# Performance work log

Hardware: AMD Instinct MI355X
Metric: run time of the kernel (lower is better)

## Reference

```python
import jax, jax.numpy as jnp
import numpy as np

N_HEADS = 16
D_HEAD = 64
N_ROTATE = 32
ROPE_BASE = 10000.0
MAX_LEN = 2048  # round_up_to_multiple_of_256(keep count); static for jit
BATCH, SEQ = 2, 4096


def setup_inputs() -> dict:
    key = jax.random.key(0)
    kq, kk, kv = jax.random.split(key, 3)
    q = jax.random.normal(kq, (BATCH, N_HEADS, MAX_LEN, D_HEAD), jnp.float32)
    k = jax.random.normal(kk, (BATCH, N_HEADS, SEQ, D_HEAD), jnp.float32)
    v = jax.random.normal(kv, (BATCH, N_HEADS, SEQ, D_HEAD), jnp.float32)
    # causal full mask [batch, seq, seq] and full position ids [batch, seq]
    mask_full = jnp.broadcast_to(jnp.tril(jnp.ones((SEQ, SEQ), bool)), (BATCH, SEQ, SEQ))
    pos_full = jnp.broadcast_to(jnp.arange(SEQ, dtype=jnp.int32), (BATCH, SEQ))
    # skip_mask: exactly MAX_LEN kept tokens per row (random positions)
    rng = np.random.default_rng(0)
    sm = np.zeros((BATCH, SEQ), dtype=bool)
    for i in range(BATCH):
        sm[i, rng.permutation(SEQ)[:MAX_LEN]] = True
    return {"q": q, "k": k, "v": v, "mask_full": mask_full,
            "pos_full": pos_full, "skip_mask": jnp.asarray(sm)}


def _rope_rotate(x, pos):
    # x: [b, h, L, n_rotate], pos: [b, L]
    half = N_ROTATE // 2
    inv_freq = 1.0 / (ROPE_BASE ** (jnp.arange(0, N_ROTATE, 2, dtype=jnp.float32) / N_ROTATE))
    freqs = pos.astype(jnp.float32)[..., None] * inv_freq          # [b, L, half]
    emb = jnp.concatenate([freqs, freqs], axis=-1)[:, None]        # [b, 1, L, n_rotate]
    cos, sin = jnp.cos(emb), jnp.sin(emb)
    x1, x2 = x[..., :half], x[..., half:]
    rot = jnp.concatenate([-x2, x1], axis=-1)                      # rotate_half
    return x * cos + rot * sin


def reference(q, k, v, mask_full, pos_full, skip_mask):
    b, S = skip_mask.shape
    lengths = skip_mask.sum(axis=1)
    # vectorized _trim_attention_mask: stable argsort compacts kept indices to the front
    order = jnp.argsort(jnp.where(skip_mask, 0, 1), axis=1, stable=True)
    idx = order[:, :MAX_LEN]                                       # [b, max_len]
    brow = jnp.arange(b)[:, None]
    mask_trim = mask_full[brow, idx]                               # [b, max_len, S]
    pos_trim = pos_full[brow, idx]                                 # [b, max_len]
    valid = jnp.arange(MAX_LEN)[None, :] < lengths[:, None]
    mask_trim = mask_trim & valid[..., None]
    pos_trim = jnp.where(valid, pos_trim, 0)

    # partial RoPE on first n_rotate channels
    rq = _rope_rotate(q[..., :N_ROTATE], pos_trim)
    rk = _rope_rotate(k[..., :N_ROTATE], pos_full)
    q = jnp.concatenate([rq, q[..., N_ROTATE:]], axis=-1)
    k = jnp.concatenate([rk, k[..., N_ROTATE:]], axis=-1)

    # masked SDPA (bool mask broadcast over heads)
    scale = 1.0 / jnp.sqrt(jnp.float32(D_HEAD))
    scores = jnp.einsum('bhqd,bhkd->bhqk', q, k) * scale
    scores = jnp.where(mask_trim[:, None], scores, jnp.finfo(scores.dtype).min)
    attn = jax.nn.softmax(scores, axis=-1)
    return jnp.einsum('bhqk,bhkd->bhqd', attn, v)
```

## Files before the change

### kernel.cpp

```cpp
#include <hip/hip_runtime.h>
#include <math.h>

#define BB 2
#define HH 16
#define QQ 2048
#define SS 4096
#define DD 64
#define NRH 16
#define NQT128 16

typedef unsigned short u16;
typedef unsigned int   u32;
typedef short bhalf8 __attribute__((ext_vector_type(8)));
typedef float f32x4  __attribute__((ext_vector_type(4)));

typedef __attribute__((address_space(1))) const u32 gu32;
typedef __attribute__((address_space(3))) u32 lu32;

#if __has_builtin(__builtin_amdgcn_exp2f)
#define EXP2(x) __builtin_amdgcn_exp2f(x)
#else
#define EXP2(x) exp2f(x)
#endif

union Frag16 { uint4 u; bhalf8 v; u16 s[8]; uint2 d[2]; };

__device__ __forceinline__ u16 f2bf(float f) {
  union { float f; u32 u; } c; c.f = f;
  return (u16)((c.u + 0x7FFFu + ((c.u >> 16) & 1u)) >> 16);
}

__device__ __forceinline__ u32 cvt_pk_bf16(float lo, float hi) {
  u32 r;
  asm("v_cvt_pk_bf16_f32 %0, %1, %2" : "=v"(r) : "v"(lo), "v"(hi));
  return r;
}

__device__ __forceinline__ bhalf8 ldfrag(const u16* p) {
  Frag16 f; f.u = *reinterpret_cast<const uint4*>(p); return f.v;
}

__device__ __forceinline__ void rope32(float* x, int pos) {
  const float step = 0.8304820237218405f;
  const float fp = (float)pos;
#pragma unroll
  for (int i = 0; i < NRH; ++i) {
    float ang = fp * exp2f(-step * (float)i);
    float sv, cv;
    __sincosf(ang, &sv, &cv);
    float a = x[i], b = x[i + NRH];
    x[i]       = a * cv - b * sv;
    x[i + NRH] = b * cv + a * sv;
  }
}

__global__ void prep_idx_kernel(const unsigned char* __restrict__ sm,
                                int* __restrict__ idx) {
  __shared__ int wsum[4];
  __shared__ int modes;
  const int tid = threadIdx.x;
  const int b = (int)blockIdx.x;

  int c = 0;
  for (int i = 0; i < 32; ++i) c += (sm[tid * 32 + i] != 0) ? 1 : 0;
#pragma unroll
  for (int off = 32; off; off >>= 1) c += __shfl_down(c, off);
  if ((tid & 63) == 0) wsum[tid >> 6] = c;
  __syncthreads();
  if (tid == 0) modes = (wsum[0] + wsum[1] + wsum[2] + wsum[3] > 3000) ? 1 : 0;
  __syncthreads();
  const bool byteMode = (modes != 0);
  const u32* sm32 = (const u32*)sm;

  const int base = b * SS + tid * 16;
  u32 flags = 0;
  for (int i = 0; i < 16; ++i) {
    bool f = byteMode ? (sm[base + i] != 0) : (sm32[base + i] != 0);
    flags |= ((u32)(f ? 1 : 0)) << i;
  }
  int cnt = __popc(flags);
  int vv = cnt;
#pragma unroll
  for (int off = 1; off < 64; off <<= 1) {
    int t = __shfl_up(vv, off);
    if ((tid & 63) >= off) vv += t;
  }
  __syncthreads();
  if ((tid & 63) == 63) wsum[tid >> 6] = vv;
  __syncthreads();
  int add = 0;
  for (int w2 = 0; w2 < (tid >> 6); ++w2) add += wsum[w2];
  int p = vv - cnt + add;
  for (int i = 0; i < 16; ++i) {
    if (flags & (1u << i)) {
      if (p < QQ) idx[b * QQ + p] = tid * 16 + i;
      ++p;
    }
  }
}

__global__ __launch_bounds__(256) void prep_kv_kernel(const float* __restrict__ k,
                                                      const float* __restrict__ v,
                                                      u16* __restrict__ kbf,
                                                      u16* __restrict__ vt) {
  __shared__ u16 tile[64][72];
  if (blockIdx.x < 512) {
    int r = blockIdx.x * 256 + threadIdx.x;
    int pos = r & (SS - 1);
    float x[64];
    const float4* src = (const float4*)(k + (size_t)r * DD);
#pragma unroll
    for (int i = 0; i < 16; ++i) {
      float4 t = src[i];
      x[4 * i] = t.x; x[4 * i + 1] = t.y; x[4 * i + 2] = t.z; x[4 * i + 3] = t.w;
    }
    rope32(x, pos);
    u16 tmp[64];
#pragma unroll
    for (int i = 0; i < 64; ++i) tmp[i] = f2bf(x[i]);
    uint4* dst = (uint4*)(kbf + (size_t)r * DD);
#pragma unroll
    for (int i = 0; i < 8; ++i) dst[i] = ((uint4*)tmp)[i];
  } else {
    int blk = (int)blockIdx.x - 512;
    int bh = blk >> 6;
    int jt = blk & 63;
    int t = threadIdx.x;
    int jl = t >> 2;
    int dc = (t & 3) * 16;
    const float4* src = (const float4*)(v + ((size_t)(bh * SS + jt * 64 + jl)) * DD + dc);
#pragma unroll
    for (int i = 0; i < 4; ++i) {
      float4 f = src[i];
      tile[jl][dc + 4 * i]     = f2bf(f.x);
      tile[jl][dc + 4 * i + 1] = f2bf(f.y);
      tile[jl][dc + 4 * i + 2] = f2bf(f.z);
      tile[jl][dc + 4 * i + 3] = f2bf(f.w);
    }
    __syncthreads();
    int d = t >> 2;
    int c = t & 3;
    u16 o[16];
#pragma unroll
    for (int m = 0; m < 16; ++m)
      o[m] = tile[4 * c + (m >> 2) + ((m & 3) << 4)][d];
    uint4* dst = (uint4*)(vt + ((size_t)(bh * DD + d)) * SS + jt * 64 + c * 16);
    dst[0] = ((uint4*)o)[0];
    dst[1] = ((uint4*)o)[1];
  }
}

__device__ __forceinline__ void stage_tiles(const char* kb_bh, const char* vt_bh,
                                            u16* Kb, u16* Vb, int t0,
                                            int w, int srow, int schk) {
#pragma unroll
  for (int p2 = 0; p2 < 2; ++p2) {
    const int rr = w * 16 + p2 * 8 + srow;
    {
      const char* g = kb_bh + (size_t)(t0 + rr) * 128 + ((schk ^ (rr & 7)) * 16);
      lu32* l = (lu32*)((char*)Kb + (w * 16 + p2 * 8) * 128);
      __builtin_amdgcn_global_load_lds((gu32*)g, l, 16, 0, 0);
    }
    {
      const char* g = vt_bh + (size_t)rr * (SS * 2) + t0 * 2 + ((schk ^ (rr & 7)) * 16);
      lu32* l = (lu32*)((char*)Vb + (w * 16 + p2 * 8) * 128);
      __builtin_amdgcn_global_load_lds((gu32*)g, l, 16, 0, 0);
    }
  }
}

template <bool MASKED>
__device__ __forceinline__ void attn_tile(
    const u16* __restrict__ Kb, const u16* __restrict__ Vb, u16* __restrict__ pb,
    int t0, int grp, int col,
    int bndA0, int bndA1, int bndA2, int bndA3,
    int bndB0, int bndB1, int bndB2, int bndB3,
    int paA0, int paA1, int paB0, int paB1,
    int pwA0, int pwA1, int pwA2, int pwA3,
    int pwB0, int pwB1, int pwB2, int pwB3,
    bhalf8 qaA0, bhalf8 qaA1, bhalf8 qaB0, bhalf8 qaB1,
    f32x4& accA0, f32x4& accA1, f32x4& accA2, f32x4& accA3,
    f32x4& accB0, f32x4& accB1, f32x4& accB2, f32x4& accB3,
    float& lA0, float& lA1, float& lA2, float& lA3,
    float& lB0, float& lB1, float& lB2, float& lB3) {
  const int swz = col & 7;
  f32x4 z = {0.f, 0.f, 0.f, 0.f};
  f32x4 sA0 = z, sA1 = z, sA2 = z, sA3 = z;
  f32x4 sB0 = z, sB1 = z, sB2 = z, sB3 = z;
  {
    const u16* kr0 = Kb + (0 * 16 + col) * 64;
    const u16* kr1 = Kb + (1 * 16 + col) * 64;
    const u16* kr2 = Kb + (2 * 16 + col) * 64;
    const u16* kr3 = Kb + (3 * 16 + col) * 64;
    __builtin_amdgcn_s_setprio(1);
    bhalf8 b0 = ldfrag(kr0 + ((grp ^ swz) * 8));
    sA0 = __builtin_amdgcn_mfma_f32_16x16x32_bf16(qaA0, b0, sA0, 0, 0, 0);
    sB0 = __builtin_amdgcn_mfma_f32_16x16x32_bf16(qaB0, b0, sB0, 0, 0, 0);
    bhalf8 b1 = ldfrag(kr1 + ((grp ^ swz) * 8));
    sA1 = __builtin_amdgcn_mfma_f32_16x16x32_bf16(qaA0, b1, sA1, 0, 0, 0);
    sB1 = __builtin_amdgcn_mfma_f32_16x16x32_bf16(qaB0, b1, sB1, 0, 0, 0);
    bhalf8 b2 = ldfrag(kr2 + ((grp ^ swz) * 8));
    sA2 = __builtin_amdgcn_mfma_f32_16x16x32_bf16(qaA0, b2, sA2, 0, 0, 0);
    sB2 = __builtin_amdgcn_mfma_f32_16x16x32_bf16(qaB0, b2, sB2, 0, 0, 0);
    bhalf8 b3 = ldfrag(kr3 + ((grp ^ swz) * 8));
    sA3 = __builtin_amdgcn_mfma_f32_16x16x32_bf16(qaA0, b3, sA3, 0, 0, 0);
    sB3 = __builtin_amdgcn_mfma_f32_16x16x32_bf16(qaB0, b3, sB3, 0, 0, 0);
    bhalf8 c0 = ldfrag(kr0 + (((4 + grp) ^ swz) * 8));
    sA0 = __builtin_amdgcn_mfma_f32_16x16x32_bf16(qaA1, c0, sA0, 0, 0, 0);
    sB0 = __builtin_amdgcn_mfma_f32_16x16x32_bf16(qaB1, c0, sB0, 0, 0, 0);
    bhalf8 c1 = ldfrag(kr1 + (((4 + grp) ^ swz) * 8));
    sA1 = __builtin_amdgcn_mfma_f32_16x16x32_bf16(qaA1, c1, sA1, 0, 0, 0);
    sB1 = __builtin_amdgcn_mfma_f32_16x16x32_bf16(qaB1, c1, sB1, 0, 0, 0);
    bhalf8 c2 = ldfrag(kr2 + (((4 + grp) ^ swz) * 8));
    sA2 = __builtin_amdgcn_mfma_f32_16x16x32_bf16(qaA1, c2, sA2, 0, 0, 0);
    sB2 = __builtin_amdgcn_mfma_f32_16x16x32_bf16(qaB1, c2, sB2, 0, 0, 0);
    bhalf8 c3 = ldfrag(kr3 + (((4 + grp) ^ swz) * 8));
    sA3 = __builtin_amdgcn_mfma_f32_16x16x32_bf16(qaA1, c3, sA3, 0, 0, 0);
    sB3 = __builtin_amdgcn_mfma_f32_16x16x32_bf16(qaB1, c3, sB3, 0, 0, 0);
    __builtin_amdgcn_s_setprio(0);
  }

  const int key0 = t0 + col;
#define SM_ROW(S0, S1, S2, S3, R, BND, LACC, PWI)                              \
  {                                                                            \
    float p0, p1, p2v, p3;                                                     \
    if (MASKED) {                                                              \
      p0  = (key0      <= (BND)) ? EXP2(S0[R] - 16.f) : 0.f;                   \
      p1  = (key0 + 16 <= (BND)) ? EXP2(S1[R] - 16.f) : 0.f;                   \
      p2v = (key0 + 32 <= (BND)) ? EXP2(S2[R] - 16.f) : 0.f;                   \
      p3  = (key0 + 48 <= (BND)) ? EXP2(S3[R] - 16.f) : 0.f;                   \
    } else {                                                                   \
      p0  = EXP2(S0[R] - 16.f);                                                \
      p1  = EXP2(S1[R] - 16.f);                                                \
      p2v = EXP2(S2[R] - 16.f);                                                \
      p3  = EXP2(S3[R] - 16.f);                                                \
    }                                                                          \
    (LACC) += (p0 + p1) + (p2v + p3);                                          \
    uint2 pw;                                                                  \
    pw.x = cvt_pk_bf16(p0, p1);                                                \
    pw.y = cvt_pk_bf16(p2v, p3);                                               \
    *(uint2*)(pb + (PWI)) = pw;                                                \
  }
  SM_ROW(sA0, sA1, sA2, sA3, 0, bndA0, lA0, pwA0)
  SM_ROW(sA0, sA1, sA2, sA3, 1, bndA1, lA1, pwA1)
  SM_ROW(sA0, sA1, sA2, sA3, 2, bndA2, lA2, pwA2)
  SM_ROW(sA0, sA1, sA2, sA3, 3, bndA3, lA3, pwA3)
  SM_ROW(sB0, sB1, sB2, sB3, 0, bndB0, lB0, pwB0)
  SM_ROW(sB0, sB1, sB2, sB3, 1, bndB1, lB1, pwB1)
  SM_ROW(sB0, sB1, sB2, sB3, 2, bndB2, lB2, pwB2)
  SM_ROW(sB0, sB1, sB2, sB3, 3, bndB3, lB3, pwB3)
#undef SM_ROW

  asm volatile("s_waitcnt lgkmcnt(0)" ::: "memory");
  __builtin_amdgcn_sched_barrier(0);

  bhalf8 paA_0, paA_1, paB_0, paB_1;
  {
    Frag16 f0, f1, g0, g1;
    f0.u = *(const uint4*)(pb + paA0);
    f1.u = *(const uint4*)(pb + paA1);
    g0.u = *(const uint4*)(pb + paB0);
    g1.u = *(const uint4*)(pb + paB1);
    paA_0 = f0.v; paA_1 = f1.v; paB_0 = g0.v; paB_1 = g1.v;
  }

  {
    const u16* vr0 = Vb + (0 * 16 + col) * 64;
    const u16* vr1 = Vb + (1 * 16 + col) * 64;
    const u16* vr2 = Vb + (2 * 16 + col) * 64;
    const u16* vr3 = Vb + (3 * 16 + col) * 64;
    __builtin_amdgcn_s_setprio(1);
    bhalf8 v0 = ldfrag(vr0 + ((grp ^ swz) * 8));
    accA0 = __builtin_amdgcn_mfma_f32_16x16x32_bf16(paA_0, v0, accA0, 0, 0, 0);
    accB0 = __builtin_amdgcn_mfma_f32_16x16x32_bf16(paB_0, v0, accB0, 0, 0, 0);
    bhalf8 v1 = ldfrag(vr1 + ((grp ^ swz) * 8));
    accA1 = __builtin_amdgcn_mfma_f32_16x16x32_bf16(paA_0, v1, accA1, 0, 0, 0);
    accB1 = __builtin_amdgcn_mfma_f32_16x16x32_bf16(paB_0, v1, accB1, 0, 0, 0);
    bhalf8 v2 = ldfrag(vr2 + ((grp ^ swz) * 8));
    accA2 = __builtin_amdgcn_mfma_f32_16x16x32_bf16(paA_0, v2, accA2, 0, 0, 0);
    accB2 = __builtin_amdgcn_mfma_f32_16x16x32_bf16(paB_0, v2, accB2, 0, 0, 0);
    bhalf8 v3 = ldfrag(vr3 + ((grp ^ swz) * 8));
    accA3 = __builtin_amdgcn_mfma_f32_16x16x32_bf16(paA_0, v3, accA3, 0, 0, 0);
    accB3 = __builtin_amdgcn_mfma_f32_16x16x32_bf16(paB_0, v3, accB3, 0, 0, 0);
    bhalf8 u0 = ldfrag(vr0 + (((4 + grp) ^ swz) * 8));
    accA0 = __builtin_amdgcn_mfma_f32_16x16x32_bf16(paA_1, u0, accA0, 0, 0, 0);
    accB0 = __builtin_amdgcn_mfma_f32_16x16x32_bf16(paB_1, u0, accB0, 0, 0, 0);
    bhalf8 u1 = ldfrag(vr1 + (((4 + grp) ^ swz) * 8));
    accA1 = __builtin_amdgcn_mfma_f32_16x16x32_bf16(paA_1, u1, accA1, 0, 0, 0);
    accB1 = __builtin_amdgcn_mfma_f32_16x16x32_bf16(paB_1, u1, accB1, 0, 0, 0);
    bhalf8 u2 = ldfrag(vr2 + (((4 + grp) ^ swz) * 8));
    accA2 = __builtin_amdgcn_mfma_f32_16x16x32_bf16(paA_1, u2, accA2, 0, 0, 0);
    accB2 = __builtin_amdgcn_mfma_f32_16x16x32_bf16(paB_1, u2, accB2, 0, 0, 0);
    bhalf8 u3 = ldfrag(vr3 + (((4 + grp) ^ swz) * 8));
    accA3 = __builtin_amdgcn_mfma_f32_16x16x32_bf16(paA_1, u3, accA3, 0, 0, 0);
    accB3 = __builtin_amdgcn_mfma_f32_16x16x32_bf16(paB_1, u3, accB3, 0, 0, 0);
    __builtin_amdgcn_s_setprio(0);
  }
}

__global__ __launch_bounds__(256) void attn_mfma_kernel(
    const float* __restrict__ qsrc, const u16* __restrict__ kbf,
    const u16* __restrict__ vt, const int* __restrict__ idx,
    float* __restrict__ out) {
  __shared__ u16 KbufA[64 * 64];
  __shared__ u16 VbufA[64 * 64];
  __shared__ u16 KbufB[64 * 64];
  __shared__ u16 VbufB[64 * 64];
  __shared__ __align__(16) u16 Pbuf[4][32 * 64];

  const int blk = (int)blockIdx.x;
  const int bh  = blk & 31;
  const int rank = blk >> 5;
  const int qt  = (rank < 8) ? (15 - 2 * rank) : (2 * (rank - 8));
  const int q0  = qt * 128;
  const int b   = bh >> 4;
  const int tid  = threadIdx.x;
  const int w    = tid >> 6;
  const int lane = tid & 63;
  const int grp  = lane >> 4;
  const int col  = lane & 15;

  const char* kb_bh = (const char*)(kbf + (size_t)bh * SS * DD);
  const char* vt_bh = (const char*)(vt + (size_t)bh * DD * SS);

  const int srow = lane >> 3;
  const int schk = lane & 7;

  u16* pb = Pbuf[w];

  const int* idxb = idx + b * QQ + q0;
  const int bndA0 = idxb[w * 32 + grp * 4 + 0];
  const int bndA1 = idxb[w * 32 + grp * 4 + 1];
  const int bndA2 = idxb[w * 32 + grp * 4 + 2];
  const int bndA3 = idxb[w * 32 + grp * 4 + 3];
  const int bndB0 = idxb[w * 32 + 16 + grp * 4 + 0];
  const int bndB1 = idxb[w * 32 + 16 + grp * 4 + 1];
  const int bndB2 = idxb[w * 32 + 16 + grp * 4 + 2];
  const int bndB3 = idxb[w * 32 + 16 + grp * 4 + 3];
  const int wave_minb = idxb[w * 32];
  const int wave_maxb = idxb[w * 32 + 31];
  const int maxbound  = idxb[127];
  const int ntiles = (maxbound >> 6) + 1;

  const int paA0 = col * 64 + ((grp ^ (col & 7)) << 3);
  const int paA1 = col * 64 + (((grp + 4) ^ (col & 7)) << 3);
  const int paB0 = (16 + col) * 64 + ((grp ^ (col & 7)) << 3);
  const int paB1 = (16 + col) * 64 + (((grp + 4) ^ (col & 7)) << 3);
  const int qg = grp * 4;
  const int pwA0 = (qg + 0) * 64 + ((((col >> 1) ^ ((qg + 0) & 7))) << 3) + ((col & 1) << 2);
  const int pwA1 = (qg + 1) * 64 + ((((col >> 1) ^ ((qg + 1) & 7))) << 3) + ((col & 1) << 2);
  const int pwA2 = (qg + 2) * 64 + ((((col >> 1) ^ ((qg + 2) & 7))) << 3) + ((col & 1) << 2);
  const int pwA3 = (qg + 3) * 64 + ((((col >> 1) ^ ((qg + 3) & 7))) << 3) + ((col & 1) << 2);
  const int pwB0 = (16 + qg + 0) * 64 + ((((col >> 1) ^ ((qg + 0) & 7))) << 3) + ((col & 1) << 2);
  const int pwB1 = (16 + qg + 1) * 64 + ((((col >> 1) ^ ((qg + 1) & 7))) << 3) + ((col & 1) << 2);
  const int pwB2 = (16 + qg + 2) * 64 + ((((col >> 1) ^ ((qg + 2) & 7))) << 3) + ((col & 1) << 2);
  const int pwB3 = (16 + qg + 3) * 64 + ((((col >> 1) ^ ((qg + 3) & 7))) << 3) + ((col & 1) << 2);

  bhalf8 qaA0, qaA1, qaB0, qaB1;
  {
    const int qrow = q0 + w * 32 + col;
    const int mypos = idx[b * QQ + qrow];
    const float* qr = qsrc + (size_t)(bh * QQ + qrow) * DD;
    const int lof = (grp & 1) * 8;
    float4 A0 = *(const float4*)(qr + lof);
    float4 A1 = *(const float4*)(qr + lof + 4);
    float4 B0 = *(const float4*)(qr + 16 + lof);
    float4 B1 = *(const float4*)(qr + 16 + lof + 4);
    float4 C0 = *(const float4*)(qr + 32 + grp * 8);
    float4 C1 = *(const float4*)(qr + 32 + grp * 8 + 4);
    float xlo[8] = {A0.x, A0.y, A0.z, A0.w, A1.x, A1.y, A1.z, A1.w};
    float xhi[8] = {B0.x, B0.y, B0.z, B0.w, B1.x, B1.y, B1.z, B1.w};
    float xq1[8] = {C0.x, C0.y, C0.z, C0.w, C1.x, C1.y, C1.z, C1.w};
    const float scq = 0.125f * 1.44269504088896f;
    const float fp = (float)mypos;
    Frag16 f0, f1;
#pragma unroll
    for (int j = 0; j < 8; ++j) {
      float ang = fp * exp2f(-0.8304820237218405f * (float)(lof + j));
      float sv, cv;
      __sincosf(ang, &sv, &cv);
      float val = (grp >= 2) ? (xhi[j] * cv + xlo[j] * sv)
                             : (xlo[j] * cv - xhi[j] * sv);
      f0.s[j] = f2bf(val * scq);
      f1.s[j] = f2bf(xq1[j] * scq);
    }
    qaA0 = f0.v; qaA1 = f1.v;
  }
  {
    const int qrow = q0 + w * 32 + 16 + col;
    const int mypos = idx[b * QQ + qrow];
    const float* qr = qsrc + (size_t)(bh * QQ + qrow) * DD;
    const int lof = (grp & 1) * 8;
    float4 A0 = *(const float4*)(qr + lof);
    float4 A1 = *(const float4*)(qr + lof + 4);
    float4 B0 = *(const float4*)(qr + 16 + lof);
    float4 B1 = *(const float4*)(qr + 16 + lof + 4);
    float4 C0 = *(const float4*)(qr + 32 + grp * 8);
    float4 C1 = *(const float4*)(qr + 32 + grp * 8 + 4);
    float xlo[8] = {A0.x, A0.y, A0.z, A0.w, A1.x, A1.y, A1.z, A1.w};
    float xhi[8] = {B0.x, B0.y, B0.z, B0.w, B1.x, B1.y, B1.z, B1.w};
    float xq1[8] = {C0.x, C0.y, C0.z, C0.w, C1.x, C1.y, C1.z, C1.w};
    const float scq = 0.125f * 1.44269504088896f;
    const float fp = (float)mypos;
    Frag16 f0, f1;
#pragma unroll
    for (int j = 0; j < 8; ++j) {
      float ang = fp * exp2f(-0.8304820237218405f * (float)(lof + j));
      float sv, cv;
      __sincosf(ang, &sv, &cv);
      float val = (grp >= 2) ? (xhi[j] * cv + xlo[j] * sv)
                             : (xlo[j] * cv - xhi[j] * sv);
      f0.s[j] = f2bf(val * scq);
      f1.s[j] = f2bf(xq1[j] * scq);
    }
    qaB0 = f0.v; qaB1 = f1.v;
  }

  f32x4 z = {0.f, 0.f, 0.f, 0.f};
  f32x4 accA0 = z, accA1 = z, accA2 = z, accA3 = z;
  f32x4 accB0 = z, accB1 = z, accB2 = z, accB3 = z;
  float lA0 = 0.f, lA1 = 0.f, lA2 = 0.f, lA3 = 0.f;
  float lB0 = 0.f, lB1 = 0.f, lB2 = 0.f, lB3 = 0.f;

#define ATTN_CALL(M, KB, VB, T0)                                               \
  attn_tile<M>(KB, VB, pb, T0, grp, col,                                       \
               bndA0, bndA1, bndA2, bndA3, bndB0, bndB1, bndB2, bndB3,         \
               paA0, paA1, paB0, paB1,                                         \
               pwA0, pwA1, pwA2, pwA3, pwB0, pwB1, pwB2, pwB3,                 \
               qaA0, qaA1, qaB0, qaB1,                                         \
               accA0, accA1, accA2, accA3, accB0, accB1, accB2, accB3,         \
               lA0, lA1, lA2, lA3, lB0, lB1, lB2, lB3)

  stage_tiles(kb_bh, vt_bh, KbufA, VbufA, 0, w, srow, schk);
  __syncthreads();

  for (int ti = 0; ti < ntiles; ti += 2) {
    const bool has1 = (ti + 1) < ntiles;
    if (has1) stage_tiles(kb_bh, vt_bh, KbufB, VbufB, (ti + 1) << 6, w, srow, schk);
    {
      const int t0 = ti << 6;
      if (t0 <= wave_maxb) {
        if (t0 + 63 <= wave_minb) ATTN_CALL(false, KbufA, VbufA, t0);
        else                      ATTN_CALL(true,  KbufA, VbufA, t0);
      }
    }
    __syncthreads();
    if (has1) {
      if (ti + 2 < ntiles)
        stage_tiles(kb_bh, vt_bh, KbufA, VbufA, (ti + 2) << 6, w, srow, schk);
      {
        const int t0 = (ti + 1) << 6;
        if (t0 <= wave_maxb) {
          if (t0 + 63 <= wave_minb) ATTN_CALL(false, KbufB, VbufB, t0);
          else                      ATTN_CALL(true,  KbufB, VbufB, t0);
        }
      }
      __syncthreads();
    }
  }
#undef ATTN_CALL

#pragma unroll
  for (int mdel = 1; mdel < 16; mdel <<= 1) {
    lA0 += __shfl_xor(lA0, mdel);
    lA1 += __shfl_xor(lA1, mdel);
    lA2 += __shfl_xor(lA2, mdel);
    lA3 += __shfl_xor(lA3, mdel);
    lB0 += __shfl_xor(lB0, mdel);
    lB1 += __shfl_xor(lB1, mdel);
    lB2 += __shfl_xor(lB2, mdel);
    lB3 += __shfl_xor(lB3, mdel);
  }
  {
    float i0 = 1.f / lA0, i1 = 1.f / lA1, i2 = 1.f / lA2, i3 = 1.f / lA3;
    float* ob = out + (size_t)(bh * QQ + q0 + w * 32 + grp * 4) * DD + col;
#pragma unroll
    for (int r = 0; r < 4; ++r) {
      float iv = (r == 0) ? i0 : (r == 1) ? i1 : (r == 2) ? i2 : i3;
      ob[(size_t)r * DD + 0]  = accA0[r] * iv;
      ob[(size_t)r * DD + 16] = accA1[r] * iv;
      ob[(size_t)r * DD + 32] = accA2[r] * iv;
      ob[(size_t)r * DD + 48] = accA3[r] * iv;
    }
  }
  {
    float i0 = 1.f / lB0, i1 = 1.f / lB1, i2 = 1.f / lB2, i3 = 1.f / lB3;
    float* ob = out + (size_t)(bh * QQ + q0 + w * 32 + 16 + grp * 4) * DD + col;
#pragma unroll
    for (int r = 0; r < 4; ++r) {
      float iv = (r == 0) ? i0 : (r == 1) ? i1 : (r == 2) ? i2 : i3;
      ob[(size_t)r * DD + 0]  = accB0[r] * iv;
      ob[(size_t)r * DD + 16] = accB1[r] * iv;
      ob[(size_t)r * DD + 32] = accB2[r] * iv;
      ob[(size_t)r * DD + 48] = accB3[r] * iv;
    }
  }
}

__global__ __launch_bounds__(64) void attn_fb_kernel(const float* __restrict__ q,
                                                     const float* __restrict__ ksrc,
                                                     const float* __restrict__ v,
                                                     const int* __restrict__ idx,
                                                     float* __restrict__ out) {
  int t = (int)(gridDim.x - 1u - blockIdx.x);
  int sub = t >> 5;
  int bh = t & 31;
  int b = bh >> 4;
  int lane = threadIdx.x;
  int qi = sub * 64 + lane;
  const int bound = idx[b * QQ + qi];

  float qreg[64];
  {
    const float4* qp = (const float4*)(q + ((size_t)bh * QQ + qi) * DD);
#pragma unroll
    for (int i = 0; i < 16; ++i) {
      float4 t4 = qp[i];
      qreg[4 * i] = t4.x; qreg[4 * i + 1] = t4.y;
      qreg[4 * i + 2] = t4.z; qreg[4 * i + 3] = t4.w;
    }
  }
  rope32(qreg, bound);
#pragma unroll
  for (int i = 0; i < 64; ++i) qreg[i] *= 0.125f;

  const float* kbase = ksrc + (size_t)bh * SS * DD;
  const float* vbase = v + (size_t)bh * SS * DD;
  float acc[64];
#pragma unroll
  for (int i = 0; i < 64; ++i) acc[i] = 0.f;
  float mrun = -INFINITY, lrun = 0.f;

  for (int j = 0; j <= bound; ++j) {
    float ka[64];
    const float4* kp = (const float4*)(kbase + (size_t)j * DD);
#pragma unroll
    for (int i = 0; i < 16; ++i) {
      float4 t4 = kp[i];
      ka[4 * i] = t4.x; ka[4 * i + 1] = t4.y;
      ka[4 * i + 2] = t4.z; ka[4 * i + 3] = t4.w;
    }
    rope32(ka, j);
    float s0 = 0.f, s1 = 0.f, s2 = 0.f, s3 = 0.f;
#pragma unroll
    for (int i = 0; i < 16; ++i) {
      s0 = fmaf(qreg[4 * i], ka[4 * i], s0);
      s1 = fmaf(qreg[4 * i + 1], ka[4 * i + 1], s1);
      s2 = fmaf(qreg[4 * i + 2], ka[4 * i + 2], s2);
      s3 = fmaf(qreg[4 * i + 3], ka[4 * i + 3], s3);
    }
    float sc = (s0 + s1) + (s2 + s3);
    if (sc > mrun) {
      float alpha = __expf(mrun - sc);
      lrun *= alpha;
#pragma unroll
      for (int i = 0; i < 64; ++i) acc[i] *= alpha;
      mrun = sc;
    }
    float pw = __expf(sc - mrun);
    lrun += pw;
    const float4* vp = (const float4*)(vbase + (size_t)j * DD);
#pragma unroll
    for (int i = 0; i < 16; ++i) {
      float4 t4 = vp[i];
      acc[4 * i] = fmaf(pw, t4.x, acc[4 * i]);
      acc[4 * i + 1] = fmaf(pw, t4.y, acc[4 * i + 1]);
      acc[4 * i + 2] = fmaf(pw, t4.z, acc[4 * i + 2]);
      acc[4 * i + 3] = fmaf(pw, t4.w, acc[4 * i + 3]);
    }
  }
  float inv = 1.0f / lrun;
  float4* op = (float4*)(out + ((size_t)bh * QQ + qi) * DD);
#pragma unroll
  for (int i = 0; i < 16; ++i) {
    float4 t4;
    t4.x = acc[4 * i] * inv; t4.y = acc[4 * i + 1] * inv;
    t4.z = acc[4 * i + 2] * inv; t4.w = acc[4 * i + 3] * inv;
    op[i] = t4;
  }
}

extern "C" void kernel_launch(void* const* d_in, const int* in_sizes, int n_in,
                              void* d_out, int out_size, void* d_ws, size_t ws_size,
                              hipStream_t stream) {
  (void)in_sizes; (void)n_in; (void)out_size;
  const float* q = (const float*)d_in[0];
  const float* k = (const float*)d_in[1];
  const float* v = (const float*)d_in[2];
  const unsigned char* skip = (const unsigned char*)d_in[5];
  float* out = (float*)d_out;

  char* base = (char*)d_ws;
  int* idx = (int*)base;
  const size_t kbytes = (size_t)BB * HH * SS * DD * 2;
  u16* kbf = (u16*)(base + 16384);
  u16* vtb = (u16*)(base + 16384 + kbytes);
  const size_t need = 16384 + 2 * kbytes;

  prep_idx_kernel<<<2, 256, 0, stream>>>(skip, idx);
  if (ws_size >= need) {
    prep_kv_kernel<<<512 + BB * HH * 64, 256, 0, stream>>>(k, v, kbf, vtb);
    attn_mfma_kernel<<<NQT128 * 32, 256, 0, stream>>>(q, kbf, vtb, idx, out);
  } else {
    attn_fb_kernel<<<1024, 64, 0, stream>>>(q, k, v, idx, out);
  }
}
```

Before: 305.0 us.

## Triple-buffer K/V tiles with explicit vmcnt waits and raw barriers

Adds a third LDS buffer pair for K/V and restructures the main loop into a rotating three-stage pipeline that prefetches two tiles ahead. Full __syncthreads is replaced by partial s_waitcnt vmcnt counts plus s_barrier, so loads for later tiles stay in flight while the current tile is computed. This relies on stage_tiles issuing direct global-to-LDS loads with a fixed count per stage, and it uses more LDS per block, which may reduce occupancy.

```diff
diff --git a/kernel.cpp b/kernel.cpp
--- a/kernel.cpp
+++ b/kernel.cpp
@@ -306,6 +306,8 @@
   __shared__ u16 VbufA[64 * 64];
   __shared__ u16 KbufB[64 * 64];
   __shared__ u16 VbufB[64 * 64];
+  __shared__ u16 KbufC[64 * 64];
+  __shared__ u16 VbufC[64 * 64];
   __shared__ __align__(16) u16 Pbuf[4][32 * 64];
 
   const int blk = (int)blockIdx.x;
@@ -431,32 +433,39 @@
                accA0, accA1, accA2, accA3, accB0, accB1, accB2, accB3,         \
                lA0, lA1, lA2, lA3, lB0, lB1, lB2, lB3)
 
-  stage_tiles(kb_bh, vt_bh, KbufA, VbufA, 0, w, srow, schk);
-  __syncthreads();
-
-  for (int ti = 0; ti < ntiles; ti += 2) {
-    const bool has1 = (ti + 1) < ntiles;
-    if (has1) stage_tiles(kb_bh, vt_bh, KbufB, VbufB, (ti + 1) << 6, w, srow, schk);
-    {
-      const int t0 = ti << 6;
-      if (t0 <= wave_maxb) {
-        if (t0 + 63 <= wave_minb) ATTN_CALL(false, KbufA, VbufA, t0);
-        else                      ATTN_CALL(true,  KbufA, VbufA, t0);
-      }
-    }
-    __syncthreads();
-    if (has1) {
-      if (ti + 2 < ntiles)
-        stage_tiles(kb_bh, vt_bh, KbufA, VbufA, (ti + 2) << 6, w, srow, schk);
-      {
-        const int t0 = (ti + 1) << 6;
-        if (t0 <= wave_maxb) {
-          if (t0 + 63 <= wave_minb) ATTN_CALL(false, KbufB, VbufB, t0);
-          else                      ATTN_CALL(true,  KbufB, VbufB, t0);
-        }
-      }
-      __syncthreads();
-    }
+  u16 *Kc0 = KbufA, *Vc0 = VbufA;
+  u16 *Kc1 = KbufB, *Vc1 = VbufB;
+  u16 *Kc2 = KbufC, *Vc2 = VbufC;
+
+  stage_tiles(kb_bh, vt_bh, Kc0, Vc0, 0, w, srow, schk);
+  if (ntiles > 1) stage_tiles(kb_bh, vt_bh, Kc1, Vc1, 64, w, srow, schk);
+
+  for (int ti = 0; ti < ntiles; ++ti) {
+    if (ti + 2 < ntiles) {
+      stage_tiles(kb_bh, vt_bh, Kc2, Vc2, (ti + 2) << 6, w, srow, schk);
+      asm volatile("s_waitcnt vmcnt(8)" ::: "memory");
+    } else if (ti + 1 < ntiles) {
+      asm volatile("s_waitcnt vmcnt(4)" ::: "memory");
+    } else {
+      asm volatile("s_waitcnt vmcnt(0)" ::: "memory");
+    }
+    __builtin_amdgcn_s_barrier();
+    asm volatile("" ::: "memory");
+
+    const int t0 = ti << 6;
+    if (t0 <= wave_maxb) {
+      if (t0 + 63 <= wave_minb) ATTN_CALL(false, Kc0, Vc0, t0);
+      else                      ATTN_CALL(true,  Kc0, Vc0, t0);
+    }
+
+    asm volatile("" ::: "memory");
+    __builtin_amdgcn_s_barrier();
+    asm volatile("" ::: "memory");
+
+    u16* tk = Kc0; u16* tv = Vc0;
+    Kc0 = Kc1; Vc0 = Vc1;
+    Kc1 = Kc2; Vc1 = Vc2;
+    Kc2 = tk;  Vc2 = tv;
   }
 #undef ATTN_CALL
 
```

Result: no change. 310.9 us (+1.9%).
